# Optimization experiments

Hardware: AMD Instinct MI355X
Metric: run time of the kernel (lower is better)

The kernel has to match this reference:

```python
import jax, jax.numpy as jnp
import numpy as np

B, T, D, H = 4, 2048, 1024, 16
S = D // H  # head dim

def setup_inputs() -> dict:
    key = jax.random.key(0)
    kx, kq, ku, kb = jax.random.split(key, 4)
    x = jax.random.normal(kx, (B, T, D), dtype=jnp.float32)
    # torch nn.Linear weights: (out, in); y = x @ W.T
    Wq = jax.random.normal(kq, (D, D), dtype=jnp.float32) * (1.0 / np.sqrt(D))
    Wu = jax.random.normal(ku, (D, D), dtype=jnp.float32) * (1.0 / np.sqrt(D))
    bu = jax.random.normal(kb, (D,), dtype=jnp.float32) * 0.01
    return {"x": x, "Wq": Wq, "Wu": Wu, "bu": bu}

def reference(x, Wq, Wu, bu):
    b, t, k = x.shape
    h, s = H, S
    # Bug in original module replicated: Q, K, V all use to_queries.
    q = x @ Wq.T  # (b,t,k)
    qh = q.reshape(b, t, h, s).transpose(0, 2, 1, 3)  # (b,h,t,s)
    scores = jnp.einsum('bhts,bhus->bhtu', qh, qh) / jnp.sqrt(jnp.asarray(s, x.dtype))
    w = jax.nn.softmax(scores, axis=-1)  # (b,h,t,t)
    out = jnp.einsum('bhtu,bhus->bhts', w, qh)  # (b,h,t,s)
    out = out.transpose(0, 2, 1, 3).reshape(b, t, k)  # merge heads
    return out @ Wu.T + bu
```

## Files before the change

### kernel.cpp

```cpp
#include <hip/hip_runtime.h>

#define B_ 4
#define T_ 2048
#define D_ 1024
#define H_ 16
#define S_ 64

typedef __attribute__((ext_vector_type(8))) short bf16x8;
typedef __attribute__((ext_vector_type(16))) float f32x16;
typedef unsigned int uint;

__device__ __forceinline__ short f2bf(float f) {
    union { float f; uint u; } v; v.f = f;
    uint r = v.u + 0x7fffu + ((v.u >> 16) & 1u);
    return (short)(r >> 16);
}

__device__ __forceinline__ void gld16(const short* g, short* l) {
    __builtin_amdgcn_global_load_lds((const __attribute__((address_space(1))) void*)g,
                                     (__attribute__((address_space(3))) void*)l, 16, 0, 0);
}

__global__ __launch_bounds__(256) void cvt3(const float* __restrict__ x,
                                            const float* __restrict__ wq,
                                            const float* __restrict__ wu,
                                            short* __restrict__ xb,
                                            short* __restrict__ wqb,
                                            short* __restrict__ wub) {
    const int NX = B_ * T_ * D_ / 8;
    const int NW = D_ * D_ / 8;
    int i = blockIdx.x * 256 + threadIdx.x;
    const float* src; short* dst; int off;
    if (i < NX)            { src = x;  dst = xb;  off = i; }
    else if (i < NX + NW)  { src = wq; dst = wqb; off = i - NX; }
    else                   { src = wu; dst = wub; off = i - NX - NW; }
    float4 a = *(const float4*)(src + (size_t)off * 8);
    float4 b = *(const float4*)(src + (size_t)off * 8 + 4);
    short o[8] = {f2bf(a.x), f2bf(a.y), f2bf(a.z), f2bf(a.w),
                  f2bf(b.x), f2bf(b.y), f2bf(b.z), f2bf(b.w)};
    *(bf16x8*)(dst + (size_t)off * 8) = *(bf16x8*)o;
}

#define STAGE_CO(t, bi) do {                                                      \
        const int kk_ = (t) << 6;                                                 \
        const short* gp_ = (wv < 4) ? Ap : Bp;                                    \
        short* lp_ = (wv < 4) ? &As[bi][0] : &Bs[bi][0];                          \
        const int wq_ = wv & 3;                                                   \
        _Pragma("unroll")                                                         \
        for (int c_ = 0; c_ < 4; ++c_) {                                          \
            const int r8_  = wq_ * 4 + c_;                 \
            const int row_ = r8_ * 8 + (lane >> 3);                               \
            const int cs_  = (lane & 7) ^ (lane >> 3);    \
            gld16(gp_ + (size_t)row_ * K + kk_ + cs_ * 8, lp_ + r8_ * 512);       \
        }                                                                         \
    } while (0)

template <bool OUT_BF16>
__global__ __launch_bounds__(512, 4) void gemm_bt(const short* __restrict__ A,
                                                  const short* __restrict__ Bt,
                                                  const float* __restrict__ bias,
                                                  void* __restrict__ Cv,
                                                  int M, int N, int K) {
    __shared__ short As[2][8192];
    __shared__ short Bs[2][8192];
    const int tid  = threadIdx.x;
    const int lane = tid & 63;
    const int wv   = tid >> 6;
    const int wm   = wv >> 1;
    const int wn   = wv & 1;
    const int h32  = lane >> 5;

    int bx = blockIdx.x, by = blockIdx.y;
    {
        const int nbx = gridDim.x, nby = gridDim.y;
        if ((nby & 7) == 0) {
            int f = blockIdx.x + nbx * blockIdx.y;
            int xcd = f & 7, slot = f >> 3;
            bx = slot % nbx;
            by = xcd * (nby >> 3) + slot / nbx;
        }
    }
    const int m0 = by * 128, n0 = bx * 128;
    const short* Ap = A + (size_t)m0 * K;
    const short* Bp = Bt + (size_t)n0 * K;

    f32x16 acc[2];
    #pragma unroll
    for (int i = 0; i < 2; ++i)
        #pragma unroll
        for (int r = 0; r < 16; ++r) acc[i][r] = 0.f;

    const int ra  = wm * 32 + (lane & 31);
    const int rb0 = wn * 64 + (lane & 31);
    const int rb1 = rb0 + 32;
    const int l7  = lane & 7;

    const int nt = K >> 6;
    STAGE_CO(0, 0);

    for (int t = 0; t < nt; ++t) {
        const int cur = t & 1;
        asm volatile("s_waitcnt vmcnt(0)" ::: "memory");
        __builtin_amdgcn_s_barrier();
        asm volatile("" ::: "memory");

        if (t + 1 < nt) STAGE_CO(t + 1, cur ^ 1);

        const short* Ab = As[cur];
        const short* Bb = Bs[cur];
        #pragma unroll
        for (int ks = 0; ks < 4; ++ks) {
            const int kk8 = ks * 2 + h32;
            const int sl  = (kk8 ^ l7) * 8;
            bf16x8 af = *(bf16x8*)&Ab[ra * 64 + sl];
            bf16x8 b0 = *(bf16x8*)&Bb[rb0 * 64 + sl];
            bf16x8 b1 = *(bf16x8*)&Bb[rb1 * 64 + sl];
            acc[0] = __builtin_amdgcn_mfma_f32_32x32x16_bf16(af, b0, acc[0], 0, 0, 0);
            acc[1] = __builtin_amdgcn_mfma_f32_32x32x16_bf16(af, b1, acc[1], 0, 0, 0);
        }
    }

    const int rbase = m0 + wm * 32;
    #pragma unroll
    for (int nt2 = 0; nt2 < 2; ++nt2) {
        const int col = n0 + wn * 64 + nt2 * 32 + (lane & 31);
        float bv = 0.f;
        if (!OUT_BF16 && bias) bv = bias[col];
        #pragma unroll
        for (int r = 0; r < 16; ++r) {
            int row = rbase + (r & 3) + 8 * (r >> 2) + 4 * h32;
            if constexpr (OUT_BF16)
                ((short*)Cv)[(size_t)row * N + col] = f2bf(acc[nt2][r]);
            else
                ((float*)Cv)[(size_t)row * N + col] = acc[nt2][r] + bv;
        }
    }
}

__global__ __launch_bounds__(256, 3) void attn_mfma(const short* __restrict__ q,
                                                    short* __restrict__ o) {
    __shared__ short smem[16384];
    const int tid  = threadIdx.x;
    const int lane = tid & 63;
    const int wv   = tid >> 6;
    const int h32  = lane >> 5;
    const int b  = blockIdx.y >> 4;
    const int hh = blockIdx.y & 15;
    const int t0 = blockIdx.x * 128;
    const short* qb = q + (size_t)b * (T_ * D_) + hh * S_;

    const int c8  = tid & 7;
    const int uu0 = tid >> 3;
    const int uu1 = uu0 + 32;
    const int u_0 = (uu0 & 0x33) | ((uu0 & 4) << 1) | ((uu0 & 8) >> 1);
    const int u_1 = (uu1 & 0x33) | ((uu1 & 4) << 1) | ((uu1 & 8) >> 1);
    const int kfo0 = (c8 * 64 + (u_0 ^ c8)) * 8;
    const int kfo1 = (c8 * 64 + (u_1 ^ c8)) * 8;
    const int kto0 = 4096 + (u_0 >> 4) * 1024 + ((u_0 >> 2) & 1) * 512 + (c8 >> 2) * 8
                   + ((u_0 & 3) | (((u_0 >> 3) & 1) << 2)) + (c8 & 3) * 16;
    const int kto1 = 4096 + (u_1 >> 4) * 1024 + ((u_1 >> 2) & 1) * 512 + (c8 >> 2) * 8
                   + ((u_1 & 3) | (((u_1 >> 3) & 1) << 2)) + (c8 & 3) * 16;
    const short* g0 = qb + (size_t)u_0 * D_ + c8 * 8;
    const short* g1 = qb + (size_t)u_1 * D_ + c8 * 8;

    bf16x8 st0 = *(const bf16x8*)g0;
    bf16x8 st1 = *(const bf16x8*)g1;
    #pragma unroll
    for (int rep = 0; rep < 4; ++rep) {
        int f = rep * 256 + tid;
        int r = f >> 3, cq = f & 7;
        bf16x8 v = *(const bf16x8*)(qb + (size_t)(t0 + r) * D_ + cq * 8);
        *(bf16x8*)&smem[(cq * 128 + (r ^ cq)) * 8] = v;
    }
    __syncthreads();
    bf16x8 Qreg[4];
    #pragma unroll
    for (int ks = 0; ks < 4; ++ks) {
        int kk8 = 2 * ks + h32;
        Qreg[ks] = *(bf16x8*)&smem[(kk8 * 128 + ((wv * 32 + (lane & 31)) ^ kk8)) * 8];
    }
    __syncthreads();
    *(bf16x8*)&smem[kfo0] = st0;
    *(bf16x8*)&smem[kfo1] = st1;
    #pragma unroll
    for (int ds = 0; ds < 8; ++ds) {
        smem[kto0 + ds * 64] = st0[ds];
        smem[kto1 + ds * 64] = st1[ds];
    }
    st0 = *(const bf16x8*)(g0 + (size_t)64 * D_);
    st1 = *(const bf16x8*)(g1 + (size_t)64 * D_);

    f32x16 accO0, accO1;
    #pragma unroll
    for (int i = 0; i < 16; ++i) { accO0[i] = 0.f; accO1[i] = 0.f; }
    float lsp0 = 0.f, lsp1 = 0.f;
    const int prow16 = ((((lane & 7) << 2) | ((lane >> 3) & 3)) * 16) + h32 * 512;
    const float SCL = 0.18033688f;

    int rb = 0;
    for (int u0 = 0; u0 < T_; u0 += 64) {
        __syncthreads();
        const int wb = rb ^ 8192;

        f32x16 aS0, aS1;
        #pragma unroll
        for (int i = 0; i < 16; ++i) { aS0[i] = 0.f; aS1[i] = 0.f; }
        __builtin_amdgcn_s_setprio(1);
        #pragma unroll
        for (int ks = 0; ks < 4; ++ks) {
            int kk8 = 2 * ks + h32;
            bf16x8 k0 = *(bf16x8*)&smem[rb + (kk8 * 64 + ((lane & 31) ^ kk8)) * 8];
            bf16x8 k1 = *(bf16x8*)&smem[rb + (kk8 * 64 + ((32 + (lane & 31)) ^ kk8)) * 8];
            aS0 = __builtin_amdgcn_mfma_f32_32x32x16_bf16(k0, Qreg[ks], aS0, 0, 0, 0);
            aS1 = __builtin_amdgcn_mfma_f32_32x32x16_bf16(k1, Qreg[ks], aS1, 0, 0, 0);
        }
        __builtin_amdgcn_s_setprio(0);

        *(bf16x8*)&smem[wb + kfo0] = st0;
        *(bf16x8*)&smem[wb + kfo1] = st1;
        #pragma unroll
        for (int ds = 0; ds < 8; ++ds) {
            smem[wb + kto0 + ds * 64] = st0[ds];
            smem[wb + kto1 + ds * 64] = st1[ds];
        }
        int un = u0 + 128; if (un >= T_) un = 0;
        st0 = *(const bf16x8*)(g0 + (size_t)un * D_);
        st1 = *(const bf16x8*)(g1 + (size_t)un * D_);

        bf16x8 af[4];
        #pragma unroll
        for (int tt = 0; tt < 2; ++tt) {
            const f32x16& a = tt ? aS1 : aS0;
            float p[16];
            #pragma unroll
            for (int r = 0; r < 16; r += 2) {
                p[r]     = __builtin_amdgcn_exp2f(a[r] * SCL);
                p[r + 1] = __builtin_amdgcn_exp2f(a[r + 1] * SCL);
                lsp0 += p[r];
                lsp1 += p[r + 1];
            }
            #pragma unroll
            for (int sub = 0; sub < 2; ++sub) {
                union { uint u[4]; bf16x8 v; } cv;
                #pragma unroll
                for (int dd = 0; dd < 4; ++dd)
                    cv.u[dd] = __builtin_amdgcn_perm(
                        __float_as_uint(p[sub * 8 + 2 * dd + 1]),
                        __float_as_uint(p[sub * 8 + 2 * dd]), 0x07060302u);
                af[tt * 2 + sub] = cv.v;
            }
        }

        __builtin_amdgcn_s_setprio(1);
        #pragma unroll
        for (int c = 0; c < 4; ++c) {
            bf16x8 v0 = *(bf16x8*)&smem[rb + 4096 + c * 1024 + prow16 + 0];
            bf16x8 v1 = *(bf16x8*)&smem[rb + 4096 + c * 1024 + prow16 + 8];
            accO0 = __builtin_amdgcn_mfma_f32_32x32x16_bf16(af[c], v0, accO0, 0, 0, 0);
            accO1 = __builtin_amdgcn_mfma_f32_32x32x16_bf16(af[c], v1, accO1, 0, 0, 0);
        }
        __builtin_amdgcn_s_setprio(0);
        rb = wb;
    }

    float lsp = lsp0 + lsp1;
    float dsum = lsp + __shfl_xor(lsp, 32);
    short* ob = o + (size_t)b * (T_ * D_) + hh * S_;
    #pragma unroll
    for (int r = 0; r < 16; ++r) {
        int rt = (r & 3) + 8 * (r >> 2) + 4 * h32;
        float inv = 1.00390625f / __shfl(dsum, rt);
        size_t t = (size_t)(t0 + wv * 32 + rt);
        ob[t * D_ + (lane & 31)]      = f2bf(accO0[r] * inv);
        ob[t * D_ + 32 + (lane & 31)] = f2bf(accO1[r] * inv);
    }
}

extern "C" void kernel_launch(void* const* d_in, const int* in_sizes, int n_in,
                              void* d_out, int out_size, void* d_ws, size_t ws_size,
                              hipStream_t stream) {
    const float* x  = (const float*)d_in[0];
    const float* Wq = (const float*)d_in[1];
    const float* Wu = (const float*)d_in[2];
    const float* bu = (const float*)d_in[3];
    float* out  = (float*)d_out;
    short* qbuf = (short*)d_out;
    short* xb   = (short*)((char*)d_out + 16777216);
    short* attn = (short*)d_ws;
    short* wqb  = (short*)((char*)d_ws + 16777216);
    short* wub  = (short*)((char*)d_ws + 18874368);

    const int M = B_ * T_;
    dim3 gg(D_ / 128, M / 128);
    hipLaunchKernelGGL(cvt3, dim3(5120), dim3(256), 0, stream, x, Wq, Wu, xb, wqb, wub);
    hipLaunchKernelGGL((gemm_bt<true>), gg, dim3(512), 0, stream,
                       xb, wqb, (const float*)nullptr, (void*)qbuf, M, D_, D_);
    hipLaunchKernelGGL(attn_mfma, dim3(T_ / 128, B_ * H_), dim3(256), 0, stream, qbuf, attn);
    hipLaunchKernelGGL((gemm_bt<false>), gg, dim3(512), 0, stream,
                       attn, wub, bu, (void*)out, M, D_, D_);
}
```

Baseline: 225.7 us.

## Use 4-wave GEMM with 64x64 warp tiles and pad attention V-transpose LDS

The projection GEMMs drop from 8 waves to 4 waves per 128x128 tile. Each wave now computes a 64x64 sub-tile with 2x2 MFMAs per k-step, so fragments are reused more and LDS reads per MFMA go down, at the cost of more accumulator registers and fewer waves to hide latency. In the attention kernel the transposed V staging area gets a padded stride (24 instead of 16 per row group), which is meant to cut LDS bank conflicts on the scalar transpose stores and the fragment loads. The padding raises the LDS footprint, and double-buffer switching now uses an offset subtraction instead of an XOR.

```diff
diff --git a/kernel.cpp b/kernel.cpp
--- a/kernel.cpp
+++ b/kernel.cpp
@@ -43,12 +43,12 @@
 
 #define STAGE_CO(t, bi) do {                                                      \
         const int kk_ = (t) << 6;                                                 \
-        const short* gp_ = (wv < 4) ? Ap : Bp;                                    \
-        short* lp_ = (wv < 4) ? &As[bi][0] : &Bs[bi][0];                          \
-        const int wq_ = wv & 3;                                                   \
+        const short* gp_ = (wv < 2) ? Ap : Bp;                                    \
+        short* lp_ = (wv < 2) ? &As[bi][0] : &Bs[bi][0];                          \
+        const int half_ = wv & 1;                                                 \
         _Pragma("unroll")                                                         \
-        for (int c_ = 0; c_ < 4; ++c_) {                                          \
-            const int r8_  = wq_ * 4 + c_;                 \
+        for (int c_ = 0; c_ < 8; ++c_) {                                          \
+            const int r8_  = half_ * 8 + c_;               \
             const int row_ = r8_ * 8 + (lane >> 3);                               \
             const int cs_  = (lane & 7) ^ (lane >> 3);    \
             gld16(gp_ + (size_t)row_ * K + kk_ + cs_ * 8, lp_ + r8_ * 512);       \
@@ -56,7 +56,7 @@
     } while (0)
 
 template <bool OUT_BF16>
-__global__ __launch_bounds__(512, 4) void gemm_bt(const short* __restrict__ A,
+__global__ __launch_bounds__(256, 2) void gemm_bt(const short* __restrict__ A,
                                                   const short* __restrict__ Bt,
                                                   const float* __restrict__ bias,
                                                   void* __restrict__ Cv,
@@ -84,15 +84,16 @@
     const short* Ap = A + (size_t)m0 * K;
     const short* Bp = Bt + (size_t)n0 * K;
 
-    f32x16 acc[2];
+    f32x16 acc[2][2];
     #pragma unroll
     for (int i = 0; i < 2; ++i)
         #pragma unroll
-        for (int r = 0; r < 16; ++r) acc[i][r] = 0.f;
-
-    const int ra  = wm * 32 + (lane & 31);
+        for (int j = 0; j < 2; ++j)
+            #pragma unroll
+            for (int r = 0; r < 16; ++r) acc[i][j][r] = 0.f;
+
+    const int ra0 = wm * 64 + (lane & 31);
     const int rb0 = wn * 64 + (lane & 31);
-    const int rb1 = rb0 + 32;
     const int l7  = lane & 7;
 
     const int nt = K >> 6;
@@ -112,34 +113,40 @@
         for (int ks = 0; ks < 4; ++ks) {
             const int kk8 = ks * 2 + h32;
             const int sl  = (kk8 ^ l7) * 8;
-            bf16x8 af = *(bf16x8*)&Ab[ra * 64 + sl];
+            bf16x8 a0 = *(bf16x8*)&Ab[ra0 * 64 + sl];
+            bf16x8 a1 = *(bf16x8*)&Ab[(ra0 + 32) * 64 + sl];
             bf16x8 b0 = *(bf16x8*)&Bb[rb0 * 64 + sl];
-            bf16x8 b1 = *(bf16x8*)&Bb[rb1 * 64 + sl];
-            acc[0] = __builtin_amdgcn_mfma_f32_32x32x16_bf16(af, b0, acc[0], 0, 0, 0);
-            acc[1] = __builtin_amdgcn_mfma_f32_32x32x16_bf16(af, b1, acc[1], 0, 0, 0);
-        }
-    }
-
-    const int rbase = m0 + wm * 32;
-    #pragma unroll
-    for (int nt2 = 0; nt2 < 2; ++nt2) {
-        const int col = n0 + wn * 64 + nt2 * 32 + (lane & 31);
-        float bv = 0.f;
-        if (!OUT_BF16 && bias) bv = bias[col];
-        #pragma unroll
-        for (int r = 0; r < 16; ++r) {
-            int row = rbase + (r & 3) + 8 * (r >> 2) + 4 * h32;
-            if constexpr (OUT_BF16)
-                ((short*)Cv)[(size_t)row * N + col] = f2bf(acc[nt2][r]);
-            else
-                ((float*)Cv)[(size_t)row * N + col] = acc[nt2][r] + bv;
+            bf16x8 b1 = *(bf16x8*)&Bb[(rb0 + 32) * 64 + sl];
+            acc[0][0] = __builtin_amdgcn_mfma_f32_32x32x16_bf16(a0, b0, acc[0][0], 0, 0, 0);
+            acc[0][1] = __builtin_amdgcn_mfma_f32_32x32x16_bf16(a0, b1, acc[0][1], 0, 0, 0);
+            acc[1][0] = __builtin_amdgcn_mfma_f32_32x32x16_bf16(a1, b0, acc[1][0], 0, 0, 0);
+            acc[1][1] = __builtin_amdgcn_mfma_f32_32x32x16_bf16(a1, b1, acc[1][1], 0, 0, 0);
+        }
+    }
+
+    #pragma unroll
+    for (int mt = 0; mt < 2; ++mt) {
+        #pragma unroll
+        for (int nt2 = 0; nt2 < 2; ++nt2) {
+            const int rbase = m0 + wm * 64 + mt * 32;
+            const int col   = n0 + wn * 64 + nt2 * 32 + (lane & 31);
+            float bv = 0.f;
+            if (!OUT_BF16 && bias) bv = bias[col];
+            #pragma unroll
+            for (int r = 0; r < 16; ++r) {
+                int row = rbase + (r & 3) + 8 * (r >> 2) + 4 * h32;
+                if constexpr (OUT_BF16)
+                    ((short*)Cv)[(size_t)row * N + col] = f2bf(acc[mt][nt2][r]);
+                else
+                    ((float*)Cv)[(size_t)row * N + col] = acc[mt][nt2][r] + bv;
+            }
         }
     }
 }
 
 __global__ __launch_bounds__(256, 3) void attn_mfma(const short* __restrict__ q,
                                                     short* __restrict__ o) {
-    __shared__ short smem[16384];
+    __shared__ short smem[20480];
     const int tid  = threadIdx.x;
     const int lane = tid & 63;
     const int wv   = tid >> 6;
@@ -156,10 +163,10 @@
     const int u_1 = (uu1 & 0x33) | ((uu1 & 4) << 1) | ((uu1 & 8) >> 1);
     const int kfo0 = (c8 * 64 + (u_0 ^ c8)) * 8;
     const int kfo1 = (c8 * 64 + (u_1 ^ c8)) * 8;
-    const int kto0 = 4096 + (u_0 >> 4) * 1024 + ((u_0 >> 2) & 1) * 512 + (c8 >> 2) * 8
-                   + ((u_0 & 3) | (((u_0 >> 3) & 1) << 2)) + (c8 & 3) * 16;
-    const int kto1 = 4096 + (u_1 >> 4) * 1024 + ((u_1 >> 2) & 1) * 512 + (c8 >> 2) * 8
-                   + ((u_1 & 3) | (((u_1 >> 3) & 1) << 2)) + (c8 & 3) * 16;
+    const int kto0 = 4096 + (u_0 >> 4) * 1536 + ((u_0 >> 2) & 1) * 768 + (c8 >> 2) * 8
+                   + ((u_0 & 3) | (((u_0 >> 3) & 1) << 2)) + (c8 & 3) * 24;
+    const int kto1 = 4096 + (u_1 >> 4) * 1536 + ((u_1 >> 2) & 1) * 768 + (c8 >> 2) * 8
+                   + ((u_1 & 3) | (((u_1 >> 3) & 1) << 2)) + (c8 & 3) * 24;
     const short* g0 = qb + (size_t)u_0 * D_ + c8 * 8;
     const short* g1 = qb + (size_t)u_1 * D_ + c8 * 8;
 
@@ -184,8 +191,8 @@
     *(bf16x8*)&smem[kfo1] = st1;
     #pragma unroll
     for (int ds = 0; ds < 8; ++ds) {
-        smem[kto0 + ds * 64] = st0[ds];
-        smem[kto1 + ds * 64] = st1[ds];
+        smem[kto0 + ds * 96] = st0[ds];
+        smem[kto1 + ds * 96] = st1[ds];
     }
     st0 = *(const bf16x8*)(g0 + (size_t)64 * D_);
     st1 = *(const bf16x8*)(g1 + (size_t)64 * D_);
@@ -194,13 +201,13 @@
     #pragma unroll
     for (int i = 0; i < 16; ++i) { accO0[i] = 0.f; accO1[i] = 0.f; }
     float lsp0 = 0.f, lsp1 = 0.f;
-    const int prow16 = ((((lane & 7) << 2) | ((lane >> 3) & 3)) * 16) + h32 * 512;
+    const int prow = ((((lane & 7) << 2) | ((lane >> 3) & 3)) * 24) + h32 * 768;
     const float SCL = 0.18033688f;
 
     int rb = 0;
     for (int u0 = 0; u0 < T_; u0 += 64) {
         __syncthreads();
-        const int wb = rb ^ 8192;
+        const int wb = 10240 - rb;
 
         f32x16 aS0, aS1;
         #pragma unroll
@@ -220,8 +227,8 @@
         *(bf16x8*)&smem[wb + kfo1] = st1;
         #pragma unroll
         for (int ds = 0; ds < 8; ++ds) {
-            smem[wb + kto0 + ds * 64] = st0[ds];
-            smem[wb + kto1 + ds * 64] = st1[ds];
+            smem[wb + kto0 + ds * 96] = st0[ds];
+            smem[wb + kto1 + ds * 96] = st1[ds];
         }
         int un = u0 + 128; if (un >= T_) un = 0;
         st0 = *(const bf16x8*)(g0 + (size_t)un * D_);
@@ -254,8 +261,8 @@
         __builtin_amdgcn_s_setprio(1);
         #pragma unroll
         for (int c = 0; c < 4; ++c) {
-            bf16x8 v0 = *(bf16x8*)&smem[rb + 4096 + c * 1024 + prow16 + 0];
-            bf16x8 v1 = *(bf16x8*)&smem[rb + 4096 + c * 1024 + prow16 + 8];
+            bf16x8 v0 = *(bf16x8*)&smem[rb + 4096 + c * 1536 + prow + 0];
+            bf16x8 v1 = *(bf16x8*)&smem[rb + 4096 + c * 1536 + prow + 8];
             accO0 = __builtin_amdgcn_mfma_f32_32x32x16_bf16(af[c], v0, accO0, 0, 0, 0);
             accO1 = __builtin_amdgcn_mfma_f32_32x32x16_bf16(af[c], v1, accO1, 0, 0, 0);
         }
@@ -293,9 +300,9 @@
     const int M = B_ * T_;
     dim3 gg(D_ / 128, M / 128);
     hipLaunchKernelGGL(cvt3, dim3(5120), dim3(256), 0, stream, x, Wq, Wu, xb, wqb, wub);
-    hipLaunchKernelGGL((gemm_bt<true>), gg, dim3(512), 0, stream,
+    hipLaunchKernelGGL((gemm_bt<true>), gg, dim3(256), 0, stream,
                        xb, wqb, (const float*)nullptr, (void*)qbuf, M, D_, D_);
     hipLaunchKernelGGL(attn_mfma, dim3(T_ / 128, B_ * H_), dim3(256), 0, stream, qbuf, attn);
-    hipLaunchKernelGGL((gemm_bt<false>), gg, dim3(512), 0, stream,
+    hipLaunchKernelGGL((gemm_bt<false>), gg, dim3(256), 0, stream,
                        attn, wub, bu, (void*)out, M, D_, D_);
 }
```

Measured after the change: 223.2 us. About the same (-1.1%).
